# Optimization experiments

Measured on AMD Instinct MI355X. Metric: run time of the kernel, lower is better.

Reference implementation:

```python
import jax, jax.numpy as jnp
import numpy as np

N_PROP = 1000
N_CLS = 81  # includes background class 0
IMG_H, IMG_W = 800, 1333
WX, WY, WW, WH = 10.0, 10.0, 5.0, 5.0
BBOX_XFORM_CLIP = float(np.log(1000.0 / 16.0))
SCORE_THRESH = 0.05
NMS_THRESH = 0.5
DET_PER_IMG = 100


def _decode(box_regression, proposals):
    widths = proposals[:, 2] - proposals[:, 0] + 1.0
    heights = proposals[:, 3] - proposals[:, 1] + 1.0
    ctr_x = proposals[:, 0] + 0.5 * widths
    ctr_y = proposals[:, 1] + 0.5 * heights
    rel = box_regression.reshape(box_regression.shape[0], -1, 4)  # [N, C, 4]
    dx = rel[..., 0] / WX
    dy = rel[..., 1] / WY
    dw = jnp.minimum(rel[..., 2] / WW, BBOX_XFORM_CLIP)
    dh = jnp.minimum(rel[..., 3] / WH, BBOX_XFORM_CLIP)
    pcx = dx * widths[:, None] + ctr_x[:, None]
    pcy = dy * heights[:, None] + ctr_y[:, None]
    pw = jnp.exp(dw) * widths[:, None]
    ph = jnp.exp(dh) * heights[:, None]
    return jnp.stack([pcx - 0.5 * pw, pcy - 0.5 * ph,
                      pcx + 0.5 * pw - 1.0, pcy + 0.5 * ph - 1.0], axis=-1)  # [N, C, 4]


def _clip_boxes(b, h, w):
    x1 = jnp.clip(b[..., 0], 0.0, w - 1.0)
    y1 = jnp.clip(b[..., 1], 0.0, h - 1.0)
    x2 = jnp.clip(b[..., 2], 0.0, w - 1.0)
    y2 = jnp.clip(b[..., 3], 0.0, h - 1.0)
    return jnp.stack([x1, y1, x2, y2], axis=-1)


def _nms_keep(boxes, scores, valid):
    # Greedy NMS for one class. boxes [N,4], scores [N], valid [N].
    # Returns keep mask in the ORIGINAL proposal order.
    n = scores.shape[0]
    order = jnp.argsort(-jnp.where(valid, scores, -jnp.inf))
    b = boxes[order]
    v = valid[order]
    x1, y1, x2, y2 = b[:, 0], b[:, 1], b[:, 2], b[:, 3]
    area = (x2 - x1 + 1.0) * (y2 - y1 + 1.0)
    iw = jnp.clip(jnp.minimum(x2[:, None], x2[None, :]) - jnp.maximum(x1[:, None], x1[None, :]) + 1.0, 0.0)
    ih = jnp.clip(jnp.minimum(y2[:, None], y2[None, :]) - jnp.maximum(y1[:, None], y1[None, :]) + 1.0, 0.0)
    inter = iw * ih
    iou = inter / (area[:, None] + area[None, :] - inter)
    idx = jnp.arange(n)

    def body(i, keep):
        sup = (iou[i] > NMS_THRESH) & (idx > i) & keep[i]
        return keep & ~sup

    keep = jax.lax.fori_loop(0, n, body, v)
    return jnp.zeros(n, dtype=bool).at[order].set(keep)


def _postprocess(class_logits, box_regression, proposal_boxes, image_h, image_w):
    prob = jax.nn.softmax(class_logits, axis=-1)             # [N, C]
    boxes = _decode(box_regression, proposal_boxes)           # [N, C, 4]
    boxes = _clip_boxes(boxes, float(image_h), float(image_w))
    scores_c = prob[:, 1:].T                                  # [C-1, N] skip background
    boxes_c = jnp.transpose(boxes[:, 1:, :], (1, 0, 2))       # [C-1, N, 4]
    valid = scores_c > SCORE_THRESH
    keep = jax.vmap(_nms_keep)(boxes_c, scores_c, valid)      # [C-1, N]
    masked = jnp.where(keep, scores_c, -jnp.inf)
    count = jnp.sum(keep)
    # torch.kthvalue(n - 100) == 101st largest kept score; keep scores >= it
    topv = jax.lax.top_k(masked.reshape(-1), DET_PER_IMG + 1)[0]
    image_thresh = jnp.where(count > DET_PER_IMG, topv[DET_PER_IMG], -jnp.inf)
    final = keep & (masked >= image_thresh)
    c1, n = scores_c.shape
    labels = jnp.broadcast_to(jnp.arange(1, c1 + 1, dtype=jnp.int32)[:, None], (c1, n))
    out_scores = jnp.where(final, scores_c, 0.0).reshape(-1)
    out_boxes = jnp.where(final[..., None], boxes_c, 0.0).reshape(-1, 4)
    out5 = jnp.concatenate([out_boxes, out_scores[:, None]], axis=1)  # [(C-1)*N, 5]
    return out5, jnp.where(final, labels, 0).reshape(-1), final.reshape(-1)


def setup_inputs() -> dict:
    key = jax.random.key(0)
    k1, k2, k3, k4 = jax.random.split(key, 4)
    # scale logits so a realistic fraction of softmax scores clears the 0.05 threshold
    class_logits = 3.0 * jax.random.normal(k1, (N_PROP, N_CLS), dtype=jnp.float32)
    box_regression = jax.random.normal(k2, (N_PROP, N_CLS * 4), dtype=jnp.float32)
    cxy = jax.random.uniform(k3, (N_PROP, 2), dtype=jnp.float32) * jnp.array([IMG_W, IMG_H], jnp.float32)
    wh = 16.0 + 284.0 * jax.random.uniform(k4, (N_PROP, 2), dtype=jnp.float32)
    x1y1 = jnp.clip(cxy - 0.5 * wh, 0.0)
    x2y2 = jnp.minimum(cxy + 0.5 * wh, jnp.array([IMG_W - 1.0, IMG_H - 1.0], jnp.float32))
    proposal_boxes = jnp.concatenate([x1y1, x2y2], axis=1)  # [N, 4] xyxy
    return {"class_logits": class_logits, "box_regression": box_regression,
            "proposal_boxes": proposal_boxes, "image_h": IMG_H, "image_w": IMG_W}


def reference(class_logits, box_regression, proposal_boxes, image_h, image_w):
    return _postprocess(class_logits, box_regression, proposal_boxes, image_h, image_w)
```

## Files before the change

### kernel.cpp

```cpp
#include <hip/hip_runtime.h>
#include <math.h>

#define N_PROP 1000
#define N_CLS  81
#define N_FG   80
#define SCORE_THRESH 0.05f
#define NMS_THRESH   0.5f
#define DET_PER_IMG  100
#define BBOX_CLIP    4.135166556742356f

#define LBL_OFF    400000
#define FIN_OFF    480000


__global__ __launch_bounds__(256)
void softmax_zero_kernel(const float* __restrict__ logits,
                         float* __restrict__ out,
                         int* __restrict__ count,
                         float* __restrict__ probT) {
    const int b = blockIdx.x;
    const int t = threadIdx.x;
    const int lane = t & 63;
    const int wave = t >> 6;
    if (b == 0 && t == 0) *count = 0;

    float4 z = make_float4(0.f, 0.f, 0.f, 0.f);
    float4* o4 = (float4*)out;
    for (int i = b * 256 + t; i < 140000; i += 250 * 256) o4[i] = z;

    const int n = b * 4 + wave;
    if (n < N_PROP) {
        const float* lrow = logits + (size_t)n * N_CLS;
        float v0 = lrow[lane];
        float v1 = (lane + 64 < N_CLS) ? lrow[lane + 64] : -INFINITY;
        float m = fmaxf(v0, v1);
        for (int off = 32; off; off >>= 1) m = fmaxf(m, __shfl_down(m, off));
        m = __shfl(m, 0);
        float e0 = expf(v0 - m);
        float e1 = (lane + 64 < N_CLS) ? expf(v1 - m) : 0.0f;
        float s = e0 + e1;
        for (int off = 32; off; off >>= 1) s += __shfl_down(s, off);
        s = __shfl(s, 0);
        if (lane >= 1)          probT[(size_t)(lane - 1) * N_PROP + n] = e0 / s;
        if (lane + 64 < N_CLS)  probT[(size_t)(lane + 63) * N_PROP + n] = e1 / s;
    }
}

__global__ __launch_bounds__(256)
void nms_kernel(const float* __restrict__ probT,
                const float* __restrict__ props,
                const float* __restrict__ reg,
                const int* __restrict__ ihp,
                const int* __restrict__ iwp,
                float* __restrict__ out,
                int* __restrict__ count,
                float* __restrict__ compact,
                int* __restrict__ svRow) {
    const int c = blockIdx.x;
    const int t = threadIdx.x;
    const int lane = t & 63;
    const int wave = t >> 6;

    __shared__ float sSc[N_PROP];
    __shared__ int   sIdx[N_PROP];
    __shared__ int   sPos[N_PROP];
    __shared__ float sx1[N_PROP], sy1[N_PROP], sx2[N_PROP], sy2[N_PROP];
    __shared__ float sar[N_PROP], sSc2[N_PROP];
    __shared__ int   sJdx[N_PROP];
    __shared__ unsigned char sKeep[N_PROP];
    __shared__ int   shV;

    for (int j = t; j < N_PROP; j += 256) sSc[j] = probT[(size_t)c * N_PROP + j];
    __syncthreads();

    if (wave == 0) {
        int V = 0;
        #pragma unroll
        for (int it = 0; it < 16; ++it) {
            int j = it * 64 + lane;
            float sc = (j < N_PROP) ? sSc[j] : -1.0f;
            bool val = (j < N_PROP) && (sc > SCORE_THRESH);
            unsigned long long mask = __ballot(val);
            int pre = __popcll(mask & ((1ULL << lane) - 1ULL));
            if (val) { sSc[V + pre] = sc; sIdx[V + pre] = j; }
            V += __popcll(mask);
        }
        if (lane == 0) shV = V;
    }
    __syncthreads();
    const int V = shV;

    for (int v = t; v < V; v += 256) {
        float s = sSc[v];
        int id = sIdx[v];
        int r = 0;
        for (int u = 0; u < V; ++u) {
            float su = sSc[u];
            r += (su > s) || (su == s && sIdx[u] < id);
        }
        sPos[v] = r;
    }
    __syncthreads();

    const float W1 = (float)iwp[0] - 1.0f;
    const float H1 = (float)ihp[0] - 1.0f;
    for (int v = t; v < V; v += 256) {
        int r = sPos[v];
        int j = sIdx[v];
        float4 pr = *(const float4*)(props + (size_t)j * 4);
        float w  = pr.z - pr.x + 1.0f;
        float h  = pr.w - pr.y + 1.0f;
        float cx = pr.x + 0.5f * w;
        float cy = pr.y + 0.5f * h;
        float4 rr = *(const float4*)(reg + ((size_t)j * N_CLS + (c + 1)) * 4);
        float dx = rr.x / 10.0f;
        float dy = rr.y / 10.0f;
        float dw = fminf(rr.z / 5.0f, BBOX_CLIP);
        float dh = fminf(rr.w / 5.0f, BBOX_CLIP);
        float pcx = dx * w + cx;
        float pcy = dy * h + cy;
        float pw = expf(dw) * w;
        float ph = expf(dh) * h;
        float bx1 = pcx - 0.5f * pw;
        float by1 = pcy - 0.5f * ph;
        float bx2 = pcx + 0.5f * pw - 1.0f;
        float by2 = pcy + 0.5f * ph - 1.0f;
        bx1 = fminf(fmaxf(bx1, 0.0f), W1);
        bx2 = fminf(fmaxf(bx2, 0.0f), W1);
        by1 = fminf(fmaxf(by1, 0.0f), H1);
        by2 = fminf(fmaxf(by2, 0.0f), H1);
        sx1[r] = bx1; sy1[r] = by1; sx2[r] = bx2; sy2[r] = by2;
        sar[r] = (bx2 - bx1 + 1.0f) * (by2 - by1 + 1.0f);
        sSc2[r] = sSc[v];
        sJdx[r] = j;
        sKeep[r] = 1;
    }
    __syncthreads();

    for (int r = 0; r < V; ++r) {
        if (sKeep[r]) {
            const float X1 = sx1[r], Y1 = sy1[r], X2 = sx2[r], Y2 = sy2[r], A = sar[r];
            for (int v = r + 1 + t; v < V; v += 256) {
                if (sKeep[v]) {
                    float iw = fminf(X2, sx2[v]) - fmaxf(X1, sx1[v]) + 1.0f;
                    float ih = fminf(Y2, sy2[v]) - fmaxf(Y1, sy1[v]) + 1.0f;
                    iw = fmaxf(iw, 0.0f);
                    ih = fmaxf(ih, 0.0f);
                    float inter = iw * ih;
                    float iou = inter / (A + sar[v] - inter);
                    if (iou > NMS_THRESH) sKeep[v] = 0;
                }
            }
        }
        __syncthreads();
    }

    for (int v = t; v < V; v += 256) {
        if (sKeep[v]) {
            size_t row = (size_t)c * N_PROP + sJdx[v];
            out[row * 5 + 0] = sx1[v];
            out[row * 5 + 1] = sy1[v];
            out[row * 5 + 2] = sx2[v];
            out[row * 5 + 3] = sy2[v];
            out[row * 5 + 4] = sSc2[v];
            int pos = atomicAdd(count, 1);
            compact[pos] = sSc2[v];
            svRow[pos] = (int)row;
        }
    }
}

__global__ __launch_bounds__(256)
void finalize_kernel(float* __restrict__ out,
                     const float* __restrict__ compact,
                     const int* __restrict__ svRow,
                     const int* __restrict__ count) {
    __shared__ float lsc[8192];
    __shared__ int red4[4];
    const int n = *count;
    const int t = threadIdx.x;
    const int lane = t & 63;
    const int wave = t >> 6;

    float th = 0.0f;
    if (n > DET_PER_IMG) {
        const bool useL = (n <= 8192);
        if (useL) {
            for (int i = t; i < n; i += 256) lsc[i] = compact[i];
            __syncthreads();
        }
        unsigned lo = 0u, hi = 0x40000000u;
        while (hi - lo > 1u) {
            unsigned mid = lo + ((hi - lo) >> 1);
            float mv = __uint_as_float(mid);
            int cnt = 0;
            if (useL) { for (int i = t; i < n; i += 256) cnt += (lsc[i] >= mv) ? 1 : 0; }
            else      { for (int i = t; i < n; i += 256) cnt += (compact[i] >= mv) ? 1 : 0; }
            for (int off = 32; off; off >>= 1) cnt += __shfl_down(cnt, off);
            if (lane == 0) red4[wave] = cnt;
            __syncthreads();
            int total = red4[0] + red4[1] + red4[2] + red4[3];
            __syncthreads();
            if (total >= DET_PER_IMG + 1) lo = mid; else hi = mid;
        }
        th = __uint_as_float(lo);
    }

    for (int i = blockIdx.x * 256 + t; i < n; i += gridDim.x * 256) {
        float sc = compact[i];
        int row = svRow[i];
        if (sc >= th) {
            int c = row / N_PROP;
            out[LBL_OFF + row] = (float)(c + 1);
            out[FIN_OFF + row] = 1.0f;
        } else {
            size_t o = (size_t)row * 5;
            out[o + 0] = 0.0f;
            out[o + 1] = 0.0f;
            out[o + 2] = 0.0f;
            out[o + 3] = 0.0f;
            out[o + 4] = 0.0f;
        }
    }
}

extern "C" void kernel_launch(void* const* d_in, const int* in_sizes, int n_in,
                              void* d_out, int out_size, void* d_ws, size_t ws_size,
                              hipStream_t stream) {
    const float* logits = (const float*)d_in[0];
    const float* reg    = (const float*)d_in[1];
    const float* props  = (const float*)d_in[2];
    const int*   ihp    = (const int*)d_in[3];
    const int*   iwp    = (const int*)d_in[4];
    float* out = (float*)d_out;

    char* ws = (char*)d_ws;
    int*   count   = (int*)(ws + 0);
    float* probT   = (float*)(ws + 64);
    float* compact = (float*)(ws + 320064);
    int*   svRow   = (int*)(ws + 640064);

    softmax_zero_kernel<<<250, 256, 0, stream>>>(logits, out, count, probT);
    nms_kernel<<<N_FG, 256, 0, stream>>>(probT, props, reg, ihp, iwp, out, count, compact, svRow);
    finalize_kernel<<<16, 256, 0, stream>>>(out, compact, svRow, count);
}
```

Before: 70.43 us.

## Use bitmask NMS and fuse top-k finalize into last NMS block

```diff
diff --git a/kernel.cpp b/kernel.cpp
--- a/kernel.cpp
+++ b/kernel.cpp
@@ -17,12 +17,13 @@
 void softmax_zero_kernel(const float* __restrict__ logits,
                          float* __restrict__ out,
                          int* __restrict__ count,
+                         int* __restrict__ done,
                          float* __restrict__ probT) {
     const int b = blockIdx.x;
     const int t = threadIdx.x;
     const int lane = t & 63;
     const int wave = t >> 6;
-    if (b == 0 && t == 0) *count = 0;
+    if (b == 0 && t == 0) { *count = 0; *done = 0; }
 
     float4 z = make_float4(0.f, 0.f, 0.f, 0.f);
     float4* o4 = (float4*)out;
@@ -54,12 +55,14 @@
                 const int* __restrict__ iwp,
                 float* __restrict__ out,
                 int* __restrict__ count,
+                int* __restrict__ done,
                 float* __restrict__ compact,
                 int* __restrict__ svRow) {
     const int c = blockIdx.x;
     const int t = threadIdx.x;
     const int lane = t & 63;
     const int wave = t >> 6;
+    const int cls = c + 1;
 
     __shared__ float sSc[N_PROP];
     __shared__ int   sIdx[N_PROP];
@@ -68,7 +71,11 @@
     __shared__ float sar[N_PROP], sSc2[N_PROP];
     __shared__ int   sJdx[N_PROP];
     __shared__ unsigned char sKeep[N_PROP];
+    __shared__ unsigned long long smask[512][8];
+    __shared__ unsigned long long skeepW[8];
     __shared__ int   shV;
+    __shared__ int   sLast;
+    __shared__ int   red4[4];
 
     for (int j = t; j < N_PROP; j += 256) sSc[j] = probT[(size_t)c * N_PROP + j];
     __syncthreads();
@@ -112,7 +119,7 @@
         float h  = pr.w - pr.y + 1.0f;
         float cx = pr.x + 0.5f * w;
         float cy = pr.y + 0.5f * h;
-        float4 rr = *(const float4*)(reg + ((size_t)j * N_CLS + (c + 1)) * 4);
+        float4 rr = *(const float4*)(reg + ((size_t)j * N_CLS + cls) * 4);
         float dx = rr.x / 10.0f;
         float dy = rr.y / 10.0f;
         float dw = fminf(rr.z / 5.0f, BBOX_CLIP);
@@ -137,65 +144,113 @@
     }
     __syncthreads();
 
-    for (int r = 0; r < V; ++r) {
-        if (sKeep[r]) {
+    if (V <= 512) {
+        const int nW = (V + 63) >> 6;
+        for (int r = t; r < V; r += 256) {
             const float X1 = sx1[r], Y1 = sy1[r], X2 = sx2[r], Y2 = sy2[r], A = sar[r];
-            for (int v = r + 1 + t; v < V; v += 256) {
-                if (sKeep[v]) {
+            for (int w = 0; w < nW; ++w) {
+                unsigned long long bits = 0ull;
+                int v0 = w << 6;
+                int vs = (r + 1 > v0) ? r + 1 : v0;
+                int ve = (V < v0 + 64) ? V : v0 + 64;
+                for (int v = vs; v < ve; ++v) {
                     float iw = fminf(X2, sx2[v]) - fmaxf(X1, sx1[v]) + 1.0f;
                     float ih = fminf(Y2, sy2[v]) - fmaxf(Y1, sy1[v]) + 1.0f;
                     iw = fmaxf(iw, 0.0f);
                     ih = fmaxf(ih, 0.0f);
                     float inter = iw * ih;
                     float iou = inter / (A + sar[v] - inter);
-                    if (iou > NMS_THRESH) sKeep[v] = 0;
+                    if (iou > NMS_THRESH) bits |= 1ull << (v - v0);
                 }
+                smask[r][w] = bits;
             }
         }
         __syncthreads();
+
+        if (t == 0) {
+            for (int w = 0; w < 8; ++w) {
+                int rem = V - (w << 6);
+                skeepW[w] = (rem >= 64) ? ~0ull : (rem <= 0 ? 0ull : ((1ull << rem) - 1ull));
+            }
+            for (int r = 0; r < V; ++r) {
+                if ((skeepW[r >> 6] >> (r & 63)) & 1ull) {
+                    for (int w = r >> 6; w < (int)((V + 63) >> 6); ++w) skeepW[w] &= ~smask[r][w];
+                }
+            }
+        }
+        __syncthreads();
+        for (int v = t; v < V; v += 256)
+            sKeep[v] = (unsigned char)((skeepW[v >> 6] >> (v & 63)) & 1ull);
+        __syncthreads();
+    } else {
+        for (int r = 0; r < V; ++r) {
+            if (sKeep[r]) {
+                const float X1 = sx1[r], Y1 = sy1[r], X2 = sx2[r], Y2 = sy2[r], A = sar[r];
+                for (int v = r + 1 + t; v < V; v += 256) {
+                    if (sKeep[v]) {
+                        float iw = fminf(X2, sx2[v]) - fmaxf(X1, sx1[v]) + 1.0f;
+                        float ih = fminf(Y2, sy2[v]) - fmaxf(Y1, sy1[v]) + 1.0f;
+                        iw = fmaxf(iw, 0.0f);
+                        ih = fmaxf(ih, 0.0f);
+                        float inter = iw * ih;
+                        float iou = inter / (A + sar[v] - inter);
+                        if (iou > NMS_THRESH) sKeep[v] = 0;
+                    }
+                }
+            }
+            __syncthreads();
+        }
     }
 
     for (int v = t; v < V; v += 256) {
         if (sKeep[v]) {
-            size_t row = (size_t)c * N_PROP + sJdx[v];
-            out[row * 5 + 0] = sx1[v];
-            out[row * 5 + 1] = sy1[v];
-            out[row * 5 + 2] = sx2[v];
-            out[row * 5 + 3] = sy2[v];
-            out[row * 5 + 4] = sSc2[v];
+            int row = c * N_PROP + sJdx[v];
+            size_t o = (size_t)row * 5;
+            out[o + 0] = sx1[v];
+            out[o + 1] = sy1[v];
+            out[o + 2] = sx2[v];
+            out[o + 3] = sy2[v];
+            out[o + 4] = sSc2[v];
+            out[LBL_OFF + row] = (float)cls;
+            out[FIN_OFF + row] = 1.0f;
             int pos = atomicAdd(count, 1);
             compact[pos] = sSc2[v];
-            svRow[pos] = (int)row;
-        }
-    }
-}
-
-__global__ __launch_bounds__(256)
-void finalize_kernel(float* __restrict__ out,
-                     const float* __restrict__ compact,
-                     const int* __restrict__ svRow,
-                     const int* __restrict__ count) {
-    __shared__ float lsc[8192];
-    __shared__ int red4[4];
-    const int n = *count;
-    const int t = threadIdx.x;
-    const int lane = t & 63;
-    const int wave = t >> 6;
+            svRow[pos] = row;
+        }
+    }
+    __syncthreads();
+
+    __threadfence();
+    if (t == 0) {
+        int old = __hip_atomic_fetch_add(done, 1, __ATOMIC_ACQ_REL, __HIP_MEMORY_SCOPE_AGENT);
+        sLast = (old == N_FG - 1) ? 1 : 0;
+    }
+    __syncthreads();
+    if (!sLast) return;
+    __threadfence();
+
+    const int n = __hip_atomic_load(count, __ATOMIC_RELAXED, __HIP_MEMORY_SCOPE_AGENT);
+    float* lsc = (float*)smask;
 
     float th = 0.0f;
+    const bool useL = (n <= 8192);
     if (n > DET_PER_IMG) {
-        const bool useL = (n <= 8192);
         if (useL) {
-            for (int i = t; i < n; i += 256) lsc[i] = compact[i];
+            for (int i = t; i < n; i += 256)
+                lsc[i] = __hip_atomic_load(&compact[i], __ATOMIC_RELAXED, __HIP_MEMORY_SCOPE_AGENT);
             __syncthreads();
         }
-        unsigned lo = 0u, hi = 0x40000000u;
+        unsigned lo = 0x3D4CCCCCu, hi = 0x40000000u;
         while (hi - lo > 1u) {
             unsigned mid = lo + ((hi - lo) >> 1);
             float mv = __uint_as_float(mid);
             int cnt = 0;
-            if (useL) { for (int i = t; i < n; i += 256) cnt += (lsc[i] >= mv) ? 1 : 0; }
-            else      { for (int i = t; i < n; i += 256) cnt += (compact[i] >= mv) ? 1 : 0; }
+            if (useL) {
+                for (int i = t; i < n; i += 256) cnt += (lsc[i] >= mv) ? 1 : 0;
+            } else {
+                for (int i = t; i < n; i += 256)
+                    cnt += (__hip_atomic_load(&compact[i], __ATOMIC_RELAXED, __HIP_MEMORY_SCOPE_AGENT) >= mv) ? 1 : 0;
+            }
             for (int off = 32; off; off >>= 1) cnt += __shfl_down(cnt, off);
             if (lane == 0) red4[wave] = cnt;
             __syncthreads();
@@ -206,20 +261,19 @@
         th = __uint_as_float(lo);
     }
 
-    for (int i = blockIdx.x * 256 + t; i < n; i += gridDim.x * 256) {
-        float sc = compact[i];
-        int row = svRow[i];
-        if (sc >= th) {
-            int c = row / N_PROP;
-            out[LBL_OFF + row] = (float)(c + 1);
-            out[FIN_OFF + row] = 1.0f;
-        } else {
+    for (int i = t; i < n; i += 256) {
+        float sc = useL ? lsc[i]
+                        : __hip_atomic_load(&compact[i], __ATOMIC_RELAXED, __HIP_MEMORY_SCOPE_AGENT);
+        if (sc < th) {
+            int row = __hip_atomic_load(&svRow[i], __ATOMIC_RELAXED, __HIP_MEMORY_SCOPE_AGENT);
             size_t o = (size_t)row * 5;
             out[o + 0] = 0.0f;
             out[o + 1] = 0.0f;
             out[o + 2] = 0.0f;
             out[o + 3] = 0.0f;
             out[o + 4] = 0.0f;
+            out[LBL_OFF + row] = 0.0f;
+            out[FIN_OFF + row] = 0.0f;
         }
     }
 }
@@ -236,11 +290,12 @@
 
     char* ws = (char*)d_ws;
     int*   count   = (int*)(ws + 0);
+    int*   done    = (int*)(ws + 4);
     float* probT   = (float*)(ws + 64);
     float* compact = (float*)(ws + 320064);
     int*   svRow   = (int*)(ws + 640064);
 
-    softmax_zero_kernel<<<250, 256, 0, stream>>>(logits, out, count, probT);
-    nms_kernel<<<N_FG, 256, 0, stream>>>(probT, props, reg, ihp, iwp, out, count, compact, svRow);
-    finalize_kernel<<<16, 256, 0, stream>>>(out, compact, svRow, count);
+    softmax_zero_kernel<<<250, 256, 0, stream>>>(logits, out, count, done, probT);
+    nms_kernel<<<N_FG, 256, 0, stream>>>(probT, props, reg, ihp, iwp,
+                                         out, count, done, compact, svRow);
 }
```

After: 74.51 us. 5.8% more time.

## Aggregate atomics per wave and single-wave threshold search in finalize

Applied to the files above, without the earlier changes.

```diff
diff --git a/kernel.cpp b/kernel.cpp
--- a/kernel.cpp
+++ b/kernel.cpp
@@ -59,7 +59,8 @@
     const int c = blockIdx.x;
     const int t = threadIdx.x;
     const int lane = t & 63;
-    const int wave = t >> 6;
+    const int cls = c + 1;
+    const unsigned long long lm = (1ull << lane) - 1ull;
 
     __shared__ float sSc[N_PROP];
     __shared__ int   sIdx[N_PROP];
@@ -73,7 +74,7 @@
     for (int j = t; j < N_PROP; j += 256) sSc[j] = probT[(size_t)c * N_PROP + j];
     __syncthreads();
 
-    if (wave == 0) {
+    if (t < 64) {
         int V = 0;
         #pragma unroll
         for (int it = 0; it < 16; ++it) {
@@ -81,8 +82,7 @@
             float sc = (j < N_PROP) ? sSc[j] : -1.0f;
             bool val = (j < N_PROP) && (sc > SCORE_THRESH);
             unsigned long long mask = __ballot(val);
-            int pre = __popcll(mask & ((1ULL << lane) - 1ULL));
-            if (val) { sSc[V + pre] = sc; sIdx[V + pre] = j; }
+            if (val) { int p = V + __popcll(mask & lm); sSc[p] = sc; sIdx[p] = j; }
             V += __popcll(mask);
         }
         if (lane == 0) shV = V;
@@ -112,7 +112,7 @@
         float h  = pr.w - pr.y + 1.0f;
         float cx = pr.x + 0.5f * w;
         float cy = pr.y + 0.5f * h;
-        float4 rr = *(const float4*)(reg + ((size_t)j * N_CLS + (c + 1)) * 4);
+        float4 rr = *(const float4*)(reg + ((size_t)j * N_CLS + cls) * 4);
         float dx = rr.x / 10.0f;
         float dy = rr.y / 10.0f;
         float dw = fminf(rr.z / 5.0f, BBOX_CLIP);
@@ -155,17 +155,27 @@
         __syncthreads();
     }
 
-    for (int v = t; v < V; v += 256) {
-        if (sKeep[v]) {
-            size_t row = (size_t)c * N_PROP + sJdx[v];
-            out[row * 5 + 0] = sx1[v];
-            out[row * 5 + 1] = sy1[v];
-            out[row * 5 + 2] = sx2[v];
-            out[row * 5 + 3] = sy2[v];
-            out[row * 5 + 4] = sSc2[v];
-            int pos = atomicAdd(count, 1);
+    for (int vb = 0; vb < V; vb += 256) {
+        int v = vb + t;
+        bool k = (v < V) && sKeep[v];
+        unsigned long long mask = __ballot(k);
+        int cntw = __popcll(mask);
+        int base = 0;
+        if (lane == 0 && cntw > 0) base = atomicAdd(count, cntw);
+        base = __shfl(base, 0);
+        if (k) {
+            int row = c * N_PROP + sJdx[v];
+            size_t o = (size_t)row * 5;
+            out[o + 0] = sx1[v];
+            out[o + 1] = sy1[v];
+            out[o + 2] = sx2[v];
+            out[o + 3] = sy2[v];
+            out[o + 4] = sSc2[v];
+            out[LBL_OFF + row] = (float)cls;
+            out[FIN_OFF + row] = 1.0f;
+            int pos = base + __popcll(mask & lm);
             compact[pos] = sSc2[v];
-            svRow[pos] = (int)row;
+            svRow[pos] = row;
         }
     }
 }
@@ -176,50 +186,50 @@
                      const int* __restrict__ svRow,
                      const int* __restrict__ count) {
     __shared__ float lsc[8192];
-    __shared__ int red4[4];
+    __shared__ float sTh;
     const int n = *count;
     const int t = threadIdx.x;
     const int lane = t & 63;
-    const int wave = t >> 6;
-
-    float th = 0.0f;
-    if (n > DET_PER_IMG) {
-        const bool useL = (n <= 8192);
-        if (useL) {
-            for (int i = t; i < n; i += 256) lsc[i] = compact[i];
-            __syncthreads();
-        }
-        unsigned lo = 0u, hi = 0x40000000u;
+
+    if (n <= DET_PER_IMG) return;
+
+    const bool useL = (n <= 8192);
+    if (useL) {
+        for (int i = t; i < n; i += 256) lsc[i] = compact[i];
+    }
+    __syncthreads();
+
+    if (t < 64) {
+        unsigned lo = 0x3D4CCCCCu, hi = 0x40000000u;
         while (hi - lo > 1u) {
             unsigned mid = lo + ((hi - lo) >> 1);
             float mv = __uint_as_float(mid);
             int cnt = 0;
-            if (useL) { for (int i = t; i < n; i += 256) cnt += (lsc[i] >= mv) ? 1 : 0; }
-            else      { for (int i = t; i < n; i += 256) cnt += (compact[i] >= mv) ? 1 : 0; }
-            for (int off = 32; off; off >>= 1) cnt += __shfl_down(cnt, off);
-            if (lane == 0) red4[wave] = cnt;
-            __syncthreads();
-            int total = red4[0] + red4[1] + red4[2] + red4[3];
-            __syncthreads();
-            if (total >= DET_PER_IMG + 1) lo = mid; else hi = mid;
-        }
-        th = __uint_as_float(lo);
-    }
+            if (useL) {
+                for (int i = lane; i < n; i += 64) cnt += (lsc[i] >= mv) ? 1 : 0;
+            } else {
+                for (int i = lane; i < n; i += 64) cnt += (compact[i] >= mv) ? 1 : 0;
+            }
+            for (int off = 32; off; off >>= 1) cnt += __shfl_xor(cnt, off);
+            if (cnt >= DET_PER_IMG + 1) lo = mid; else hi = mid;
+        }
+        if (lane == 0) sTh = __uint_as_float(lo);
+    }
+    __syncthreads();
+    const float th = sTh;
 
     for (int i = blockIdx.x * 256 + t; i < n; i += gridDim.x * 256) {
         float sc = compact[i];
-        int row = svRow[i];
-        if (sc >= th) {
-            int c = row / N_PROP;
-            out[LBL_OFF + row] = (float)(c + 1);
-            out[FIN_OFF + row] = 1.0f;
-        } else {
+        if (sc < th) {
+            int row = svRow[i];
             size_t o = (size_t)row * 5;
             out[o + 0] = 0.0f;
             out[o + 1] = 0.0f;
             out[o + 2] = 0.0f;
             out[o + 3] = 0.0f;
             out[o + 4] = 0.0f;
+            out[LBL_OFF + row] = 0.0f;
+            out[FIN_OFF + row] = 0.0f;
         }
     }
 }
@@ -241,6 +251,7 @@
     int*   svRow   = (int*)(ws + 640064);
 
     softmax_zero_kernel<<<250, 256, 0, stream>>>(logits, out, count, probT);
-    nms_kernel<<<N_FG, 256, 0, stream>>>(probT, props, reg, ihp, iwp, out, count, compact, svRow);
+    nms_kernel<<<N_FG, 256, 0, stream>>>(probT, props, reg, ihp, iwp,
+                                         out, count, compact, svRow);
     finalize_kernel<<<16, 256, 0, stream>>>(out, compact, svRow, count);
 }
```

After: 70.28 us. Within noise of the previous version (-0.2%).
